# Performance work log

Measured on AMD Instinct MI355X. Metric: run time of the kernel, lower is better.

The kernel has to match this reference:

```python
import jax, jax.numpy as jnp
import numpy as np

B, T, H = 4, 4096, 2048
G_EPS = 0.5
LN_EPS = 1e-5
INIT_STD = 0.02


def setup_inputs() -> dict:
    key = jax.random.key(0)
    ks = jax.random.split(key, 4)
    return {
        "hidden_states": jax.random.normal(ks[0], (B, T, H), jnp.float32),
        "W_z": jax.random.normal(ks[1], (H, H), jnp.float32) * INIT_STD,
        "b_z": jnp.zeros((H,), jnp.float32),
        "W_h": jax.random.normal(ks[2], (H, H), jnp.float32) * INIT_STD,
        "b_h": jnp.zeros((H,), jnp.float32),
        "ln_w": jnp.ones((H,), jnp.float32),
        "ln_b": jnp.zeros((H,), jnp.float32),
        "h0": jax.random.normal(ks[3], (H,), jnp.float32) * INIT_STD,
    }


def _g_log(x):
    # torch.where(x >= 0, log(relu(x) + g_eps), -softplus(-x))
    return jnp.where(x >= 0, jnp.log(jax.nn.relu(x) + G_EPS), -jax.nn.softplus(-x))


def reference(hidden_states, W_z, b_z, W_h, b_h, ln_w, ln_b, h0):
    Bc, Tc, Hc = hidden_states.shape
    k = hidden_states @ W_z.T + b_z                      # [B,T,H]
    log_z = -jax.nn.softplus(-k)                         # log sigmoid(k)
    log_coeffs = -jax.nn.softplus(k)                     # log(1 - sigmoid(k))
    log_tilde_h = _g_log(hidden_states @ W_h.T + b_h)    # [B,T,H]
    log_h0 = jnp.broadcast_to(_g_log(h0), (Bc, 1, Hc))
    log_values = jnp.concatenate([log_h0, log_z + log_tilde_h], axis=1)  # [B,T+1,H]
    # NOTE: faithful to source: cumsum over the LAST (hidden) dim, then pad one
    # zero row at the front of the time dim (F.pad(..., (0,0,1,0))).
    a_star = jnp.pad(jnp.cumsum(log_coeffs, axis=-1), ((0, 0), (1, 0), (0, 0)))  # [B,T+1,H]
    log_h = a_star + jax.lax.cumlogsumexp(log_values - a_star, axis=1)
    # global mean / unbiased std normalization, as in source
    log_h = (log_h - log_h.mean()) / jnp.std(log_h, ddof=1)
    h = jnp.exp(log_h)[:, 1:, :]                         # drop the h0 step
    # residual + LayerNorm (dropout is identity in eval)
    x = h + hidden_states
    mu = x.mean(axis=-1, keepdims=True)
    var = x.var(axis=-1, keepdims=True)
    return (x - mu) * jax.lax.rsqrt(var + LN_EPS) * ln_w + ln_b
```

## Files before the change

### kernel.cpp

```cpp
#include <hip/hip_runtime.h>
#include <stdint.h>

constexpr int NB = 4;
constexpr int NT = 4096;
constexpr int NH = 2048;
constexpr int MROWS = NB * NT;
constexpr int TP1 = NT + 1;
constexpr int CH2 = 17;
constexpr int NCH2 = 241;
constexpr int NKT = NH / 64;

typedef unsigned short u16;
typedef __bf16 bf16x8 __attribute__((ext_vector_type(8)));
typedef float f32x4 __attribute__((ext_vector_type(4)));
typedef unsigned short u16x8 __attribute__((ext_vector_type(8)));
typedef _Float16 h16x8 __attribute__((ext_vector_type(8)));
typedef u16x8 __attribute__((may_alias)) u16x8_a;
typedef h16x8 __attribute__((may_alias)) h16x8_a;
typedef float4 __attribute__((may_alias)) float4_a;

__device__ __forceinline__ u16 f2bf(float f) {
  unsigned int u = __float_as_uint(f);
  return (u16)((u + 0x7fffu + ((u >> 16) & 1u)) >> 16);
}
__device__ __forceinline__ float bf2f(u16 v) {
  return __uint_as_float(((unsigned int)v) << 16);
}
__device__ __forceinline__ float spf_(float x) {
  return fmaxf(x, 0.f) + __logf(1.f + __expf(-fabsf(x)));
}
__device__ __forceinline__ float glogf_(float x) {
  return (x >= 0.f) ? __logf(x + 0.5f) : -spf_(-x);
}
__device__ __forceinline__ void gld16(const void* g, void* l) {
  __builtin_amdgcn_global_load_lds((const __attribute__((address_space(1))) void*)g,
                                   (__attribute__((address_space(3))) void*)l, 16, 0, 0);
}
__device__ __forceinline__ void ld8(const float* p, float* r) {
  float4 a = *(const float4_a*)p, b = *(const float4_a*)(p + 4);
  r[0] = a.x; r[1] = a.y; r[2] = a.z; r[3] = a.w;
  r[4] = b.x; r[5] = b.y; r[6] = b.z; r[7] = b.w;
}
__device__ __forceinline__ void st8(float* p, const float* r) {
  *(float4_a*)p       = make_float4(r[0], r[1], r[2], r[3]);
  *(float4_a*)(p + 4) = make_float4(r[4], r[5], r[6], r[7]);
}

__global__ __launch_bounds__(256) void cvt_all(
    const float* __restrict__ hs, const float* __restrict__ Wz,
    const float* __restrict__ Wh, u16* __restrict__ hsb,
    u16* __restrict__ wzb, u16* __restrict__ whb) {
  const int s0 = MROWS * NH / 8;
  const int s1 = s0 + NH * NH / 8;
  const int s2 = s1 + NH * NH / 8;
  int i = blockIdx.x * 256 + threadIdx.x;
  if (i >= s2) return;
  const float* in; u16* out; int j;
  if (i < s0)      { in = hs; out = hsb; j = i; }
  else if (i < s1) { in = Wz; out = wzb; j = i - s0; }
  else             { in = Wh; out = whb; j = i - s1; }
  const float4* p = (const float4*)in;
  float4 a = p[2 * (size_t)j], b = p[2 * (size_t)j + 1];
  u16x8 o;
  o[0] = f2bf(a.x); o[1] = f2bf(a.y); o[2] = f2bf(a.z); o[3] = f2bf(a.w);
  o[4] = f2bf(b.x); o[5] = f2bf(b.y); o[6] = f2bf(b.z); o[7] = f2bf(b.w);
  *(u16x8*)(out + (size_t)j * 8) = o;
}

__global__ __launch_bounds__(256, 2) void gemm_db(
    const u16* __restrict__ A,
    const u16* __restrict__ Bz, const u16* __restrict__ Bh,
    const float* __restrict__ bz, const float* __restrict__ bh,
    u16* __restrict__ KU) {
  const u16* Bm  = blockIdx.y ? Bh : Bz;
  const float* bias = blockIdx.y ? bh : bz;
  u16* Cw = KU + (blockIdx.y ? 2048 : 0);

  const int bid = blockIdx.x;
  const int wg = (bid & 7) * 256 + (bid >> 3);
  const int bx = wg & 15;
  const int by = wg >> 4;
  const int row0 = by << 7, col0 = bx << 7;

  __shared__ u16 ldsA[2][128 * 64];
  __shared__ u16 ldsB[2][128 * 64];

  const int tid = threadIdx.x;
  const int lane = tid & 63;
  const int wv = tid >> 6;
  const int wr = (wv >> 1) << 6;
  const int wc = (wv & 1) << 6;

  const int srow = lane >> 3;
  const int sslot = ((lane & 7) ^ srow) << 3;
  const int xsw = (lane & 7) << 3;
  const int q8 = (lane >> 4) << 3;
  const int f15 = lane & 15;

#define STAGE(sb, k0)                                                          \
  _Pragma("unroll")                                                            \
  for (int i_ = 0; i_ < 4; ++i_) {                                             \
    const int r_ = i_ * 32 + wv * 8 + srow;                                    \
    const size_t gc_ = (size_t)((k0) + sslot);                                 \
    gld16(A  + (size_t)(row0 + r_) * NH + gc_,                                 \
          &ldsA[sb][(size_t)(i_ * 256 + wv * 64) * 8]);                        \
    gld16(Bm + (size_t)(col0 + r_) * NH + gc_,                                 \
          &ldsB[sb][(size_t)(i_ * 256 + wv * 64) * 8]);                        \
  }

  f32x4 acc[4][4] = {};

  STAGE(0, 0);
  __syncthreads();

  int cur = 0;
  for (int t = 0; t < NKT; ++t) {
    if (t + 1 < NKT) { STAGE(cur ^ 1, (t + 1) << 6); }
    __builtin_amdgcn_sched_barrier(0);
    const u16* la = ldsA[cur];
    const u16* lb = ldsB[cur];
#pragma unroll
    for (int ks = 0; ks < 2; ++ks) {
      const int cphys = ((ks << 5) | q8) ^ xsw;
      bf16x8 af[4], bfr[4];
#pragma unroll
      for (int m = 0; m < 4; ++m)
        af[m] = *(const bf16x8*)&la[(wr + m * 16 + f15) * 64 + cphys];
#pragma unroll
      for (int n = 0; n < 4; ++n)
        bfr[n] = *(const bf16x8*)&lb[(wc + n * 16 + f15) * 64 + cphys];
#pragma unroll
      for (int m = 0; m < 4; ++m)
#pragma unroll
        for (int n = 0; n < 4; ++n)
          acc[m][n] = __builtin_amdgcn_mfma_f32_16x16x32_bf16(af[m], bfr[n], acc[m][n], 0, 0, 0);
    }
    __syncthreads();
    cur ^= 1;
  }
#undef STAGE

  const int fr = lane & 15, fq = lane >> 4;
#pragma unroll
  for (int n = 0; n < 4; ++n) {
    const int col = col0 + wc + n * 16 + fr;
    const float bv = bias[col];
#pragma unroll
    for (int m = 0; m < 4; ++m) {
#pragma unroll
      for (int v = 0; v < 4; ++v) {
        const int row = row0 + wr + m * 16 + fq * 4 + v;
        Cw[(size_t)row * 4096 + col] = f2bf(acc[m][n][v] + bv);
      }
    }
  }
}

__device__ __forceinline__ void row_pointwise(const char* KU, size_t row,
                                              int tid, float* lc, float* lv) {
  const size_t rb = row * 8192;
  u16x8 kv = *(const u16x8_a*)(KU + rb + tid * 16);
  u16x8 uv = *(const u16x8_a*)(KU + rb + 4096 + tid * 16);
#pragma unroll
  for (int e = 0; e < 8; ++e) {
    const float k = bf2f(kv[e]);
    const float L = __logf(1.f + __expf(-fabsf(k)));
    lc[e] = -fmaxf(k, 0.f) - L;
    lv[e] = fminf(k, 0.f) - L + glogf_(bf2f(uv[e]));
  }
}

__global__ __launch_bounds__(256) void carry_pass(
    const char* __restrict__ KU, float* __restrict__ cm, float* __restrict__ cs,
    const float* __restrict__ h0) {
  const int ch = blockIdx.x;
  const int b = blockIdx.y;
  const int tid = threadIdx.x;
  const int lane = tid & 63, wvx = tid >> 6;
  const int t0 = ch * CH2;
  const int t1 = (t0 + CH2 < TP1) ? (t0 + CH2) : TP1;

  float m8[8], s8[8];
#pragma unroll
  for (int e = 0; e < 8; ++e) { m8[e] = -INFINITY; s8[e] = 0.f; }

  __shared__ float wsum[2][4];

  float lc[8], lv[8];
  {
    const int tf = (t0 < 1) ? 1 : t0;
    if (tf < t1) row_pointwise(KU, (size_t)b * NT + (tf - 1), tid, lc, lv);
  }

  for (int tt = t0; tt < t1; ++tt) {
    if (tt == 0) {
#pragma unroll
      for (int e = 0; e < 8; ++e) {
        const float x = glogf_(h0[tid * 8 + e]);
        m8[e] = x; s8[e] = 1.f;
      }
      continue;
    }
    float nlc[8], nlv[8];
    const bool pf = (tt + 1 < t1);
    if (pf) row_pointwise(KU, (size_t)b * NT + tt, tid, nlc, nlv);

    float cum[8], run = 0.f;
#pragma unroll
    for (int e = 0; e < 8; ++e) { run += lc[e]; cum[e] = run; }
    float v = run;
#pragma unroll
    for (int d = 1; d < 64; d <<= 1) {
      float o = __shfl_up(v, d, 64);
      if (lane >= d) v += o;
    }
    const int par = tt & 1;
    if (lane == 63) wsum[par][wvx] = v;
    __syncthreads();
    float base = v - run;
#pragma unroll
    for (int w = 0; w < 4; ++w)
      if (w < wvx) base += wsum[par][w];

#pragma unroll
    for (int e = 0; e < 8; ++e) {
      const float x = lv[e] - (base + cum[e]);
      const float nm = fmaxf(m8[e], x);
      s8[e] = s8[e] * __expf(m8[e] - nm) + __expf(x - nm);
      m8[e] = nm;
    }
    if (pf) {
#pragma unroll
      for (int e = 0; e < 8; ++e) { lc[e] = nlc[e]; lv[e] = nlv[e]; }
    }
  }
  const size_t co = ((size_t)ch * NB + b) * NH + tid * 8;
  st8(cm + co, m8);
  st8(cs + co, s8);
}

__global__ __launch_bounds__(256) void carryscan(float* __restrict__ cm,
                                                 float* __restrict__ cs) {
  const int c = blockIdx.x * 256 + threadIdx.x;
  const int b = c >> 11;
  const int hh = c & (NH - 1);
  float Cm = -INFINITY, Cs = 0.f;
  size_t o = ((size_t)0 * NB + b) * NH + hh;
  float m2 = cm[o], s2 = cs[o];
  for (int ch = 0; ch < NCH2; ++ch) {
    float nm2, ns2;
    if (ch + 1 < NCH2) {
      const size_t on = ((size_t)(ch + 1) * NB + b) * NH + hh;
      nm2 = cm[on]; ns2 = cs[on];
    }
    cm[o] = Cm; cs[o] = Cs;
    const float M = fmaxf(Cm, m2);
    Cs = Cs * __expf(Cm - M) + s2 * __expf(m2 - M);
    Cm = M;
    o = ((size_t)(ch + 1) * NB + b) * NH + hh;
    m2 = nm2; s2 = ns2;
  }
}

template <int HLH>
__global__ __launch_bounds__(256) void scan_final(
    const char* __restrict__ KU, float* __restrict__ LH32,
    _Float16* __restrict__ LH16,
    const float* __restrict__ cm, const float* __restrict__ cs,
    const float* __restrict__ h0, double* __restrict__ sums) {
  const int ch = blockIdx.x;
  const int b = blockIdx.y;
  const int tid = threadIdx.x;
  const int lane = tid & 63, wvx = tid >> 6;
  const int t0 = ch * CH2;
  const int t1 = (t0 + CH2 < TP1) ? (t0 + CH2) : TP1;

  float m8[8], s8[8];
  {
    const size_t co = ((size_t)ch * NB + b) * NH + tid * 8;
    ld8(cm + co, m8);
    ld8(cs + co, s8);
  }

  __shared__ float wsum[2][4];
  double s1 = 0.0, s2 = 0.0;

  float lc[8], lv[8];
  {
    const int tf = (t0 < 1) ? 1 : t0;
    if (tf < t1) row_pointwise(KU, (size_t)b * NT + (tf - 1), tid, lc, lv);
  }

  for (int tt = t0; tt < t1; ++tt) {
    if (tt == 0) {
#pragma unroll
      for (int e = 0; e < 8; ++e) {
        const float x = glogf_(h0[tid * 8 + e]);
        m8[e] = x; s8[e] = 1.f;
        s1 += (double)x;
        s2 += (double)x * (double)x;
      }
      continue;
    }
    float nlc[8], nlv[8];
    const bool pf = (tt + 1 < t1);
    if (pf) row_pointwise(KU, (size_t)b * NT + tt, tid, nlc, nlv);

    float cum[8], run = 0.f;
#pragma unroll
    for (int e = 0; e < 8; ++e) { run += lc[e]; cum[e] = run; }
    float v = run;
#pragma unroll
    for (int d = 1; d < 64; d <<= 1) {
      float o = __shfl_up(v, d, 64);
      if (lane >= d) v += o;
    }
    const int par = tt & 1;
    if (lane == 63) wsum[par][wvx] = v;
    __syncthreads();
    float base = v - run;
#pragma unroll
    for (int w = 0; w < 4; ++w)
      if (w < wvx) base += wsum[par][w];

    float lh8[8];
#pragma unroll
    for (int e = 0; e < 8; ++e) {
      const float as = base + cum[e];
      const float x = lv[e] - as;
      const float nm = fmaxf(m8[e], x);
      s8[e] = s8[e] * __expf(m8[e] - nm) + __expf(x - nm);
      m8[e] = nm;
      const float lh = as + nm + __logf(s8[e]);
      lh8[e] = lh;
      s1 += (double)lh;
      s2 += (double)lh * (double)lh;
    }
    const size_t row = (size_t)b * NT + (tt - 1);
    if (HLH) {
      h16x8 hv;
#pragma unroll
      for (int e = 0; e < 8; ++e) hv[e] = (_Float16)lh8[e];
      *(h16x8_a*)(LH16 + row * NH + tid * 8) = hv;
    } else {
      st8(LH32 + row * NH + tid * 8, lh8);
    }
    if (pf) {
#pragma unroll
      for (int e = 0; e < 8; ++e) { lc[e] = nlc[e]; lv[e] = nlv[e]; }
    }
  }
  double v1 = s1, v2 = s2;
#pragma unroll
  for (int d = 32; d; d >>= 1) {
    v1 += __shfl_down(v1, d, 64);
    v2 += __shfl_down(v2, d, 64);
  }
  __shared__ double dr1[4], dr2[4];
  if (lane == 0) { dr1[wvx] = v1; dr2[wvx] = v2; }
  __syncthreads();
  if (tid == 0) {
    atomicAdd(&sums[0], dr1[0] + dr1[1] + dr1[2] + dr1[3]);
    atomicAdd(&sums[1], dr2[0] + dr2[1] + dr2[2] + dr2[3]);
  }
}

__global__ void finalize_stats(const double* __restrict__ sums,
                               float* __restrict__ stats) {
  const double S = sums[0], S2 = sums[1];
  const double N = (double)NB * (double)TP1 * (double)NH;
  const double mu = S / N;
  const double var = (S2 - S * S / N) / (N - 1.0);
  stats[0] = (float)mu;
  stats[1] = (float)(1.0 / sqrt(var));
}

template <int HLH>
__global__ __launch_bounds__(256) void final_ln(
    float* __restrict__ OUT, const float* __restrict__ LH32,
    const _Float16* __restrict__ LH16, const u16* __restrict__ hsb,
    const float* __restrict__ lnw, const float* __restrict__ lnb,
    const float* __restrict__ stats) {
  const int tid = threadIdx.x;
  const size_t off = (size_t)blockIdx.x * NH + tid * 8;
  const float mu_g = stats[0], isd = stats[1];

  float lh[8], av[8];
  if (HLH) {
    h16x8 hv = *(const h16x8_a*)(LH16 + off);
#pragma unroll
    for (int e = 0; e < 8; ++e) lh[e] = (float)hv[e];
  } else {
    ld8(LH32 + off, lh);
  }
  {
    u16x8 hv = *(const u16x8_a*)(hsb + off);
#pragma unroll
    for (int e = 0; e < 8; ++e) av[e] = bf2f(hv[e]);
  }
  float x[8];
  float s = 0.f, q = 0.f;
#pragma unroll
  for (int e = 0; e < 8; ++e) {
    x[e] = __expf((lh[e] - mu_g) * isd) + av[e];
    s += x[e];
    q += x[e] * x[e];
  }
#pragma unroll
  for (int d = 32; d; d >>= 1) {
    s += __shfl_down(s, d, 64);
    q += __shfl_down(q, d, 64);
  }
  __shared__ float r1[4], r2[4];
  const int lane = tid & 63, wvx = tid >> 6;
  if (lane == 0) { r1[wvx] = s; r2[wvx] = q; }
  __syncthreads();
  const float st = r1[0] + r1[1] + r1[2] + r1[3];
  const float qt = r2[0] + r2[1] + r2[2] + r2[3];
  const float mean = st * (1.0f / NH);
  const float var = qt * (1.0f / NH) - mean * mean;
  const float rstd = rsqrtf(var + 1e-5f);

  float wv8[8], bv8[8];
  ld8(lnw + tid * 8, wv8);
  ld8(lnb + tid * 8, bv8);
  float o[8];
#pragma unroll
  for (int e = 0; e < 8; ++e)
    o[e] = (x[e] - mean) * rstd * wv8[e] + bv8[e];
  st8(OUT + off, o);
}

extern "C" void kernel_launch(void* const* d_in, const int* in_sizes, int n_in,
                              void* d_out, int out_size, void* d_ws, size_t ws_size,
                              hipStream_t stream) {
  (void)in_sizes; (void)n_in; (void)out_size;
  const float* hs  = (const float*)d_in[0];
  const float* Wz  = (const float*)d_in[1];
  const float* bz  = (const float*)d_in[2];
  const float* Wh  = (const float*)d_in[3];
  const float* bh  = (const float*)d_in[4];
  const float* lnw = (const float*)d_in[5];
  const float* lnb = (const float*)d_in[6];
  const float* h0  = (const float*)d_in[7];
  float* out = (float*)d_out;

  char* w0 = (char*)d_ws;
  char* w = w0;
  u16* hsb   = (u16*)w;  w += (size_t)MROWS * NH * 2;
  u16* wzb   = (u16*)w;  w += (size_t)NH * NH * 2;
  u16* whb   = (u16*)w;  w += (size_t)NH * NH * 2;
  char* KU   = w;        w += (size_t)MROWS * 8192;
  double* sums = (double*)w; w += 16;
  float* stats = (float*)w;  w += 64;
  _Float16* LH16 = (_Float16*)w;
  const size_t need_half = (size_t)(w - w0) + (size_t)MROWS * NH * 2;
  const bool use_half = (ws_size >= need_half);
  float* cm_ = (float*)wzb;
  float* cs_ = cm_ + (size_t)NCH2 * NB * NH;

  hipMemsetAsync(sums, 0, 16, stream);

  {
    const int tot8 = MROWS * NH / 8 + 2 * (NH * NH / 8);
    cvt_all<<<dim3((tot8 + 255) / 256), 256, 0, stream>>>(hs, Wz, Wh, hsb, wzb, whb);
  }

  gemm_db<<<dim3((MROWS / 128) * (NH / 128), 2), 256, 0, stream>>>(
      hsb, wzb, whb, bz, bh, (u16*)KU);

  carry_pass<<<dim3(NCH2, NB), 256, 0, stream>>>(KU, cm_, cs_, h0);

  carryscan<<<dim3(NB * NH / 256), 256, 0, stream>>>(cm_, cs_);

  if (use_half)
    scan_final<1><<<dim3(NCH2, NB), 256, 0, stream>>>(KU, out, LH16, cm_, cs_, h0, sums);
  else
    scan_final<0><<<dim3(NCH2, NB), 256, 0, stream>>>(KU, out, LH16, cm_, cs_, h0, sums);
  finalize_stats<<<1, 1, 0, stream>>>(sums, stats);

  if (use_half)
    final_ln<1><<<dim3(MROWS), 256, 0, stream>>>(out, out, LH16, hsb, lnw, lnb, stats);
  else
    final_ln<0><<<dim3(MROWS), 256, 0, stream>>>(out, out, LH16, hsb, lnw, lnb, stats);
}
```

Measured before the change: 580.9 us.

## Single-buffer GEMM for higher occupancy and parallelize carry scan across wave lanes

The GEMM drops its LDS double buffer in favour of a single buffer with load-then-sync per k-step, and raises launch bounds to 3 blocks per CU to hide latency through occupancy instead of prefetch. The carry scan changes from one serial 241-step loop per thread to one wavefront per (batch, hidden) column, using a shuffle-based parallel log-sum-exp prefix over chunks in four 64-wide segments. The scan gains parallelism but its column-strided accesses are now spread across lanes and less coalesced. The GEMM loses its load/compute overlap and becomes exposed to global-load latency at each step.

```diff
diff --git a/kernel.cpp b/kernel.cpp
--- a/kernel.cpp
+++ b/kernel.cpp
@@ -8,7 +8,6 @@
 constexpr int TP1 = NT + 1;
 constexpr int CH2 = 17;
 constexpr int NCH2 = 241;
-constexpr int NKT = NH / 64;
 
 typedef unsigned short u16;
 typedef __bf16 bf16x8 __attribute__((ext_vector_type(8)));
@@ -44,6 +43,12 @@
 __device__ __forceinline__ void st8(float* p, const float* r) {
   *(float4_a*)p       = make_float4(r[0], r[1], r[2], r[3]);
   *(float4_a*)(p + 4) = make_float4(r[4], r[5], r[6], r[7]);
+}
+__device__ __forceinline__ void lsecomb(float& M, float& S, float Mo, float So) {
+  const float Mn = fmaxf(M, Mo);
+  float Sn = S * __expf(M - Mn) + So * __expf(Mo - Mn);
+  if (Mn == -INFINITY) Sn = 0.f;
+  M = Mn; S = Sn;
 }
 
 __global__ __launch_bounds__(256) void cvt_all(
@@ -67,7 +72,7 @@
   *(u16x8*)(out + (size_t)j * 8) = o;
 }
 
-__global__ __launch_bounds__(256, 2) void gemm_db(
+__global__ __launch_bounds__(256, 3) void gemm_bt(
     const u16* __restrict__ A,
     const u16* __restrict__ Bz, const u16* __restrict__ Bh,
     const float* __restrict__ bz, const float* __restrict__ bh,
@@ -82,8 +87,8 @@
   const int by = wg >> 4;
   const int row0 = by << 7, col0 = bx << 7;
 
-  __shared__ u16 ldsA[2][128 * 64];
-  __shared__ u16 ldsB[2][128 * 64];
+  __shared__ u16 ldsA[128 * 64];
+  __shared__ u16 ldsB[128 * 64];
 
   const int tid = threadIdx.x;
   const int lane = tid & 63;
@@ -97,48 +102,35 @@
   const int q8 = (lane >> 4) << 3;
   const int f15 = lane & 15;
 
-#define STAGE(sb, k0)                                                          \
-  _Pragma("unroll")                                                            \
-  for (int i_ = 0; i_ < 4; ++i_) {                                             \
-    const int r_ = i_ * 32 + wv * 8 + srow;                                    \
-    const size_t gc_ = (size_t)((k0) + sslot);                                 \
-    gld16(A  + (size_t)(row0 + r_) * NH + gc_,                                 \
-          &ldsA[sb][(size_t)(i_ * 256 + wv * 64) * 8]);                        \
-    gld16(Bm + (size_t)(col0 + r_) * NH + gc_,                                 \
-          &ldsB[sb][(size_t)(i_ * 256 + wv * 64) * 8]);                        \
-  }
-
   f32x4 acc[4][4] = {};
 
-  STAGE(0, 0);
-  __syncthreads();
-
-  int cur = 0;
-  for (int t = 0; t < NKT; ++t) {
-    if (t + 1 < NKT) { STAGE(cur ^ 1, (t + 1) << 6); }
-    __builtin_amdgcn_sched_barrier(0);
-    const u16* la = ldsA[cur];
-    const u16* lb = ldsB[cur];
+  for (int k0 = 0; k0 < NH; k0 += 64) {
+    if (k0) __syncthreads();
+#pragma unroll
+    for (int i = 0; i < 4; ++i) {
+      const int r = i * 32 + wv * 8 + srow;
+      const size_t gcol = (size_t)(k0 + sslot);
+      gld16(A  + (size_t)(row0 + r) * NH + gcol, &ldsA[(size_t)(i * 256 + wv * 64) * 8]);
+      gld16(Bm + (size_t)(col0 + r) * NH + gcol, &ldsB[(size_t)(i * 256 + wv * 64) * 8]);
+    }
+    __syncthreads();
 #pragma unroll
     for (int ks = 0; ks < 2; ++ks) {
       const int cphys = ((ks << 5) | q8) ^ xsw;
       bf16x8 af[4], bfr[4];
 #pragma unroll
       for (int m = 0; m < 4; ++m)
-        af[m] = *(const bf16x8*)&la[(wr + m * 16 + f15) * 64 + cphys];
+        af[m] = *(const bf16x8*)&ldsA[(wr + m * 16 + f15) * 64 + cphys];
 #pragma unroll
       for (int n = 0; n < 4; ++n)
-        bfr[n] = *(const bf16x8*)&lb[(wc + n * 16 + f15) * 64 + cphys];
+        bfr[n] = *(const bf16x8*)&ldsB[(wc + n * 16 + f15) * 64 + cphys];
 #pragma unroll
       for (int m = 0; m < 4; ++m)
 #pragma unroll
         for (int n = 0; n < 4; ++n)
           acc[m][n] = __builtin_amdgcn_mfma_f32_16x16x32_bf16(af[m], bfr[n], acc[m][n], 0, 0, 0);
     }
-    __syncthreads();
-    cur ^= 1;
-  }
-#undef STAGE
+  }
 
   const int fr = lane & 15, fq = lane >> 4;
 #pragma unroll
@@ -241,24 +233,36 @@
 
 __global__ __launch_bounds__(256) void carryscan(float* __restrict__ cm,
                                                  float* __restrict__ cs) {
-  const int c = blockIdx.x * 256 + threadIdx.x;
+  const int wvx = threadIdx.x >> 6, lane = threadIdx.x & 63;
+  const int c = blockIdx.x * 4 + wvx;
   const int b = c >> 11;
   const int hh = c & (NH - 1);
   float Cm = -INFINITY, Cs = 0.f;
-  size_t o = ((size_t)0 * NB + b) * NH + hh;
-  float m2 = cm[o], s2 = cs[o];
-  for (int ch = 0; ch < NCH2; ++ch) {
-    float nm2, ns2;
-    if (ch + 1 < NCH2) {
-      const size_t on = ((size_t)(ch + 1) * NB + b) * NH + hh;
-      nm2 = cm[on]; ns2 = cs[on];
-    }
-    cm[o] = Cm; cs[o] = Cs;
-    const float M = fmaxf(Cm, m2);
-    Cs = Cs * __expf(Cm - M) + s2 * __expf(m2 - M);
-    Cm = M;
-    o = ((size_t)(ch + 1) * NB + b) * NH + hh;
-    m2 = nm2; s2 = ns2;
+#pragma unroll
+  for (int s = 0; s < 4; ++s) {
+    const int idx = s * 64 + lane;
+    const bool val = (idx < NCH2);
+    size_t o = 0;
+    float M = -INFINITY, S = 0.f;
+    if (val) {
+      o = ((size_t)idx * NB + b) * NH + hh;
+      M = cm[o]; S = cs[o];
+    }
+#pragma unroll
+    for (int d = 1; d < 64; d <<= 1) {
+      const float Mo = __shfl_up(M, d, 64);
+      const float So = __shfl_up(S, d, 64);
+      if (lane >= d) lsecomb(M, S, Mo, So);
+    }
+    float Me = __shfl_up(M, 1, 64);
+    float Se = __shfl_up(S, 1, 64);
+    if (lane == 0) { Me = -INFINITY; Se = 0.f; }
+    float Om = Cm, Os = Cs;
+    lsecomb(Om, Os, Me, Se);
+    if (val) { cm[o] = Om; cs[o] = Os; }
+    const float Mt = __shfl(M, 63, 64);
+    const float St = __shfl(S, 63, 64);
+    lsecomb(Cm, Cs, Mt, St);
   }
 }
 
@@ -466,12 +470,12 @@
     cvt_all<<<dim3((tot8 + 255) / 256), 256, 0, stream>>>(hs, Wz, Wh, hsb, wzb, whb);
   }
 
-  gemm_db<<<dim3((MROWS / 128) * (NH / 128), 2), 256, 0, stream>>>(
+  gemm_bt<<<dim3((MROWS / 128) * (NH / 128), 2), 256, 0, stream>>>(
       hsb, wzb, whb, bz, bh, (u16*)KU);
 
   carry_pass<<<dim3(NCH2, NB), 256, 0, stream>>>(KU, cm_, cs_, h0);
 
-  carryscan<<<dim3(NB * NH / 256), 256, 0, stream>>>(cm_, cs_);
+  carryscan<<<dim3(NB * NH / 4), 256, 0, stream>>>(cm_, cs_);
 
   if (use_half)
     scan_final<1><<<dim3(NCH2, NB), 256, 0, stream>>>(KU, out, LH16, cm_, cs_, h0, sums);
```

Result: slower. 599.1 us (+3.1%).
